# Optimization experiments

Measured on AMD Instinct MI355X. Metric: run time of the kernel, lower is better.

The kernel has to match this reference:

```python
import jax, jax.numpy as jnp
from jax import lax
import numpy as np

P, N, C, S = 16, 128, 256, 64
HID = C // 4  # squeeze_ratio = 4
NEG_SLOPE = 0.01  # nn.LeakyReLU default


def setup_inputs() -> dict:
    key = jax.random.key(0)
    k = jax.random.split(key, 5)
    sc = 0.05
    return {
        "x": jax.random.normal(k[0], (P, N, C, S), jnp.float32),
        "w1a": jax.random.normal(k[1], (P, HID, C, 3), jnp.float32) * sc,
        "w1b": jax.random.normal(k[2], (P, C, HID, 1), jnp.float32) * sc,
        "w3a": jax.random.normal(k[3], (P, HID, C, 3), jnp.float32) * sc,
        "w3b": jax.random.normal(k[4], (P, C, HID, 3), jnp.float32) * sc,
    }


def _conv1d(x, w, pad):
    # x: [n, c_in, s], w: [c_out, c_in, k] -> [n, c_out, s]
    return lax.conv_general_dilated(
        x, w, window_strides=(1,), padding=[(pad, pad)],
        dimension_numbers=("NCH", "OIH", "NCH"))


def _leaky(z):
    return jnp.where(z >= 0, z, NEG_SLOPE * z)


def _avg_pool(x, k, pad):
    # PyTorch AvgPool1d default count_include_pad=True: divide by k everywhere.
    s = lax.reduce_window(x, 0.0, lax.add, (1, 1, k), (1, 1, 1),
                          [(0, 0), (0, 0), (pad, pad)])
    return s / k


def _max_pool(x, k, pad):
    return lax.reduce_window(x, -jnp.inf, lax.max, (1, 1, k), (1, 1, 1),
                             [(0, 0), (0, 0), (pad, pad)])


def reference(x, w1a, w1b, w3a, w3b):
    p, n, c, s = x.shape
    xf = x.reshape(p * n, c, s)

    # 3x1 branch: per-part Conv1d(c->hid,k3,p1) -> LeakyReLU -> Conv1d(hid->c,k1,p0)
    logits3x1 = jax.vmap(
        lambda xi, a, b: _conv1d(_leaky(_conv1d(xi, a, 1)), b, 0))(x, w1a, w1b)
    feat3x1 = (_avg_pool(xf, 3, 1) + _max_pool(xf, 3, 1)).reshape(p, n, c, s)
    feat3x1 = feat3x1 * jax.nn.sigmoid(logits3x1)

    # 3x3 branch: per-part Conv1d(c->hid,k3,p1) -> LeakyReLU -> Conv1d(hid->c,k3,p1)
    logits3x3 = jax.vmap(
        lambda xi, a, b: _conv1d(_leaky(_conv1d(xi, a, 1)), b, 1))(x, w3a, w3b)
    feat3x3 = (_avg_pool(xf, 5, 2) + _max_pool(xf, 5, 2)).reshape(p, n, c, s)
    feat3x3 = feat3x3 * jax.nn.sigmoid(logits3x3)

    # fused temporal max over s -> [p, n, c]
    return jnp.max(feat3x1 + feat3x3, axis=-1)
```

## Files before the change

### kernel.cpp

```cpp
#include <hip/hip_runtime.h>

#define PARTS 16
#define NB 128
#define CH 256
#define SL 64
#define HIDN 64

typedef unsigned short u16;
typedef unsigned short ushort8 __attribute__((ext_vector_type(8)));
typedef unsigned short ushort4v __attribute__((ext_vector_type(4)));
typedef __attribute__((ext_vector_type(8))) short short8v;
typedef __attribute__((ext_vector_type(4))) short short4v;
typedef __attribute__((ext_vector_type(4))) float f32x4;

__device__ __forceinline__ float bf2f(u16 u) {
  union { unsigned u; float f; } t; t.u = ((unsigned)u) << 16; return t.f;
}
__device__ __forceinline__ u16 f2bf(float f) {
  union { float f; unsigned u; } t; t.f = f;
  unsigned u = t.u;
  u += 0x7FFFu + ((u >> 16) & 1u);
  return (u16)(u >> 16);
}

__global__ void cvt_tap(const float* __restrict__ in, u16* __restrict__ out, int NT) {
  const int i = blockIdx.x * 256 + threadIdx.x;
  const int p = i >> 14, xid = i & 16383;
  const float* src = in + (size_t)i * NT;
  for (int t = 0; t < NT; ++t)
    out[(size_t)(p * NT + t) * 16384 + xid] = f2bf(src[t]);
}

#define XROWS 68
#define HROWS 66

__device__ __forceinline__ int xsw(int r, int c) { return (r * 256 + c) ^ ((r & 7) << 3); }
__device__ __forceinline__ int hsw(int r, int c) { return (r * 64 + c) ^ ((r & 7) << 3); }

__global__ __launch_bounds__(256, 2) void tfa_mfma(
    const float* __restrict__ x,
    const u16* __restrict__ wsb,
    float* __restrict__ out)
{
  const u16* W1A = wsb;
  const u16* W3A = wsb + 786432;
  const u16* W1B = wsb + 1572864;
  const u16* W3B = wsb + 1835008;

  __shared__ __attribute__((aligned(16))) u16 xt[XROWS * 256];
  __shared__ __attribute__((aligned(16))) u16 ht1[HROWS * 64];
  __shared__ __attribute__((aligned(16))) u16 ht3[HROWS * 64];

  const int tid = threadIdx.x;
  const int bid = blockIdx.x;
  const int p = bid >> 7;
  const int lane = tid & 63;
  const int w = tid >> 6;

  if (tid < 128) {
    const int rr4 = (tid >> 5);
    const int r = (rr4 == 0) ? 0 : (rr4 == 1) ? 1 : (rr4 == 2) ? 66 : 67;
    const int c = (tid & 31) * 8;
    *(ushort8*)&xt[xsw(r, c)] = (ushort8)0;
  } else if (tid < 160) {
    const int t2 = tid - 128;
    const int r = (t2 & 8) ? 65 : 0;
    const int c = (t2 & 7) * 8;
    u16* b = (t2 & 16) ? ht3 : ht1;
    *(ushort8*)&b[hsw(r, c)] = (ushort8)0;
  }

  {
    const float* xb = x + (size_t)bid * (CH * SL);
    const int s = lane;
    const int r = s + 2;
    #pragma unroll
    for (int j = 0; j < 8; ++j) {
      const int c0 = w * 64 + j * 8;
      ushort8 ov;
      #pragma unroll
      for (int k = 0; k < 8; ++k) ov[k] = f2bf(xb[(c0 + k) * 64 + s]);
      *(ushort8*)&xt[xsw(r, c0)] = ov;
    }
  }
  __syncthreads();

  {
    const int hm = lane & 15;
    const int kg = lane >> 4;
    const int h = w * 16 + hm;
    f32x4 acc1[4], acc3[4];
    #pragma unroll
    for (int nt = 0; nt < 4; ++nt) { acc1[nt] = (f32x4)0.f; acc3[nt] = (f32x4)0.f; }

    #pragma unroll 2
    for (int ks = 0; ks < 8; ++ks) {
      const int kc = ks * 32 + kg * 8;
      short8v a1[3], a3[3];
      #pragma unroll
      for (int t = 0; t < 3; ++t) {
        a1[t] = *(const short8v*)&W1A[(size_t)((p * 3 + t) * 64 + h) * 256 + kc];
        a3[t] = *(const short8v*)&W3A[(size_t)((p * 3 + t) * 64 + h) * 256 + kc];
      }
      #pragma unroll
      for (int nt = 0; nt < 4; ++nt) {
        const int s = nt * 16 + hm;
        #pragma unroll
        for (int t = 0; t < 3; ++t) {
          const int r = s + t + 1;
          const short8v b = *(const short8v*)&xt[xsw(r, kc)];
          acc1[nt] = __builtin_amdgcn_mfma_f32_16x16x32_bf16(a1[t], b, acc1[nt], 0, 0, 0);
          acc3[nt] = __builtin_amdgcn_mfma_f32_16x16x32_bf16(a3[t], b, acc3[nt], 0, 0, 0);
        }
      }
    }

    const int hc = w * 16 + kg * 4;
    #pragma unroll
    for (int nt = 0; nt < 4; ++nt) {
      const int s = nt * 16 + hm;
      const int r = s + 1;
      ushort4v o1, o3;
      #pragma unroll
      for (int q = 0; q < 4; ++q) {
        float v1 = acc1[nt][q]; v1 = v1 >= 0.f ? v1 : 0.01f * v1;
        float v3 = acc3[nt][q]; v3 = v3 >= 0.f ? v3 : 0.01f * v3;
        o1[q] = f2bf(v1); o3[q] = f2bf(v3);
      }
      *(ushort4v*)&ht1[hsw(r, hc)] = o1;
      *(ushort4v*)&ht3[hsw(r, hc)] = o3;
    }
  }
  __syncthreads();

  {
    const int cm = lane & 15;
    const int kg = lane >> 4;

    #pragma unroll
    for (int half = 0; half < 2; ++half) {
      const int mtb = half * 2;
      f32x4 acc[2][4];
      #pragma unroll
      for (int mt = 0; mt < 2; ++mt)
        #pragma unroll
        for (int nt = 0; nt < 4; ++nt) acc[mt][nt] = (f32x4)0.f;

      #pragma unroll
      for (int ks = 0; ks < 2; ++ks) {
        const int kh = ks * 32 + kg * 8;
        short8v a[2];
        #pragma unroll
        for (int mt = 0; mt < 2; ++mt) {
          const int c = w * 64 + (mtb + mt) * 16 + cm;
          a[mt] = *(const short8v*)&W1B[((size_t)p * 256 + c) * 64 + kh];
        }
        #pragma unroll
        for (int nt = 0; nt < 4; ++nt) {
          const int s = nt * 16 + cm;
          const short8v b = *(const short8v*)&ht1[hsw(s + 1, kh)];
          #pragma unroll
          for (int mt = 0; mt < 2; ++mt)
            acc[mt][nt] = __builtin_amdgcn_mfma_f32_16x16x32_bf16(a[mt], b, acc[mt][nt], 0, 0, 0);
        }
      }

      unsigned g1p[2][4][2];
      #pragma unroll
      for (int mt = 0; mt < 2; ++mt)
        #pragma unroll
        for (int nt = 0; nt < 4; ++nt) {
          #pragma unroll
          for (int j = 0; j < 2; ++j) {
            const float ga = 1.f / (1.f + __expf(-acc[mt][nt][2 * j]));
            const float gb = 1.f / (1.f + __expf(-acc[mt][nt][2 * j + 1]));
            g1p[mt][nt][j] = (unsigned)f2bf(ga) | ((unsigned)f2bf(gb) << 16);
          }
          acc[mt][nt] = (f32x4)0.f;
        }

      #pragma unroll
      for (int ks = 0; ks < 2; ++ks) {
        const int kh = ks * 32 + kg * 8;
        #pragma unroll
        for (int t = 0; t < 3; ++t) {
          short8v a[2];
          #pragma unroll
          for (int mt = 0; mt < 2; ++mt) {
            const int c = w * 64 + (mtb + mt) * 16 + cm;
            a[mt] = *(const short8v*)&W3B[(size_t)((p * 3 + t) * 256 + c) * 64 + kh];
          }
          #pragma unroll
          for (int nt = 0; nt < 4; ++nt) {
            const int s = nt * 16 + cm;
            const short8v b = *(const short8v*)&ht3[hsw(s + t, kh)];
            #pragma unroll
            for (int mt = 0; mt < 2; ++mt)
              acc[mt][nt] = __builtin_amdgcn_mfma_f32_16x16x32_bf16(a[mt], b, acc[mt][nt], 0, 0, 0);
          }
        }
      }

      #pragma unroll
      for (int mt = 0; mt < 2; ++mt) {
        const int c4 = w * 64 + (mtb + mt) * 16 + kg * 4;
        float fmx0 = -INFINITY, fmx1 = -INFINITY, fmx2 = -INFINITY, fmx3 = -INFINITY;
        #pragma unroll
        for (int nt = 0; nt < 4; ++nt) {
          const int s = nt * 16 + cm;
          const ushort4v vm2 = *(const ushort4v*)&xt[xsw(s,     c4)];
          const ushort4v vm1 = *(const ushort4v*)&xt[xsw(s + 1, c4)];
          const ushort4v v0  = *(const ushort4v*)&xt[xsw(s + 2, c4)];
          const ushort4v vp1 = *(const ushort4v*)&xt[xsw(s + 3, c4)];
          const ushort4v vp2 = *(const ushort4v*)&xt[xsw(s + 4, c4)];
          const float NI = -INFINITY;
          float ft[4];
          #pragma unroll
          for (int q = 0; q < 4; ++q) {
            const float xm2 = bf2f(vm2[q]), xm1 = bf2f(vm1[q]), x0 = bf2f(v0[q]);
            const float xp1 = bf2f(vp1[q]), xp2 = bf2f(vp2[q]);
            const float mx3 = fmaxf(x0, fmaxf(s >= 1 ? xm1 : NI, s <= 62 ? xp1 : NI));
            const float mx5 = fmaxf(mx3, fmaxf(s >= 2 ? xm2 : NI, s <= 61 ? xp2 : NI));
            const float av3 = (xm1 + x0 + xp1) * (1.f / 3.f);
            const float av5 = (xm2 + xm1 + x0 + xp1 + xp2) * 0.2f;
            const float g1 = bf2f((u16)(g1p[mt][nt][q >> 1] >> ((q & 1) * 16)));
            const float g3 = 1.f / (1.f + __expf(-acc[mt][nt][q]));
            ft[q] = (av3 + mx3) * g1 + (av5 + mx5) * g3;
          }
          fmx0 = fmaxf(fmx0, ft[0]); fmx1 = fmaxf(fmx1, ft[1]);
          fmx2 = fmaxf(fmx2, ft[2]); fmx3 = fmaxf(fmx3, ft[3]);
        }
        #pragma unroll
        for (int off = 1; off < 16; off <<= 1) {
          fmx0 = fmaxf(fmx0, __shfl_xor(fmx0, off));
          fmx1 = fmaxf(fmx1, __shfl_xor(fmx1, off));
          fmx2 = fmaxf(fmx2, __shfl_xor(fmx2, off));
          fmx3 = fmaxf(fmx3, __shfl_xor(fmx3, off));
        }
        if (cm == 0) {
          float4 o; o.x = fmx0; o.y = fmx1; o.z = fmx2; o.w = fmx3;
          *(float4*)&out[(size_t)bid * 256 + c4] = o;
        }
      }
    }
  }
}

#define XROW 72
#define HROW 72

__global__ __launch_bounds__(256, 2) void tfa_kernel(
    const float* __restrict__ x,
    const float* __restrict__ w1a,
    const float* __restrict__ w1b,
    const float* __restrict__ w3a,
    const float* __restrict__ w3b,
    float* __restrict__ out)
{
  __shared__ __attribute__((aligned(16))) u16 x_s[8 + CH * XROW];
  __shared__ __attribute__((aligned(16))) u16 h1_s[8 + HIDN * HROW];
  __shared__ __attribute__((aligned(16))) u16 h3_s[8 + HIDN * HROW];

  const int tid = threadIdx.x;
  const int bid = blockIdx.x;
  const int p = bid >> 7;

  {
    const ushort8 z = {0, 0, 0, 0, 0, 0, 0, 0};
    for (int i = tid; i < 257; i += 256) {
      u16* dst = (i == 0) ? &x_s[0] : &x_s[8 + (i - 1) * XROW + 64];
      *(ushort8*)dst = z;
    }
    if (tid < 65) {
      u16* d1 = (tid == 0) ? &h1_s[0] : &h1_s[8 + (tid - 1) * HROW + 64];
      *(ushort8*)d1 = z;
      u16* d3 = (tid == 0) ? &h3_s[0] : &h3_s[8 + (tid - 1) * HROW + 64];
      *(ushort8*)d3 = z;
    }
  }

  const float* xblk = x + (size_t)bid * (CH * SL);
  #pragma unroll
  for (int j = 0; j < 16; ++j) {
    const int g = tid + 256 * j;
    const float4 v = ((const float4*)xblk)[g];
    const int c = g >> 4, s4 = g & 15;
    ushort4v o;
    o[0] = f2bf(v.x); o[1] = f2bf(v.y); o[2] = f2bf(v.z); o[3] = f2bf(v.w);
    *(ushort4v*)&x_s[8 + c * XROW + s4 * 4] = o;
  }
  __syncthreads();

  {
    const int h = tid >> 2;
    const int sg = tid & 3;
    const int sb = sg << 4;
    float acc1[16], acc3[16];
    #pragma unroll
    for (int i = 0; i < 16; ++i) { acc1[i] = 0.f; acc3[i] = 0.f; }

    const float* w1a_p = w1a + ((size_t)p * HIDN + h) * (CH * 3);
    const float* w3a_p = w3a + ((size_t)p * HIDN + h) * (CH * 3);

    for (int c4 = 0; c4 < CH; c4 += 4) {
      const float4 a0v = *(const float4*)&w1a_p[c4 * 3];
      const float4 a1v = *(const float4*)&w1a_p[c4 * 3 + 4];
      const float4 a2v = *(const float4*)&w1a_p[c4 * 3 + 8];
      const float4 b0v = *(const float4*)&w3a_p[c4 * 3];
      const float4 b1v = *(const float4*)&w3a_p[c4 * 3 + 4];
      const float4 b2v = *(const float4*)&w3a_p[c4 * 3 + 8];
      float wa[12], wb[12];
      wa[0]=a0v.x; wa[1]=a0v.y; wa[2]=a0v.z; wa[3]=a0v.w;
      wa[4]=a1v.x; wa[5]=a1v.y; wa[6]=a1v.z; wa[7]=a1v.w;
      wa[8]=a2v.x; wa[9]=a2v.y; wa[10]=a2v.z; wa[11]=a2v.w;
      wb[0]=b0v.x; wb[1]=b0v.y; wb[2]=b0v.z; wb[3]=b0v.w;
      wb[4]=b1v.x; wb[5]=b1v.y; wb[6]=b1v.z; wb[7]=b1v.w;
      wb[8]=b2v.x; wb[9]=b2v.y; wb[10]=b2v.z; wb[11]=b2v.w;

      #pragma unroll
      for (int cc = 0; cc < 4; ++cc) {
        const int c = c4 + cc;
        const ushort8 w0v = *(const ushort8*)&x_s[c * XROW + sb];
        const ushort8 w1v = *(const ushort8*)&x_s[c * XROW + sb + 8];
        const ushort8 w2v = *(const ushort8*)&x_s[c * XROW + sb + 16];
        const ushort8 w3v = *(const ushort8*)&x_s[c * XROW + sb + 24];
        float xf[19];
        xf[0] = bf2f(w0v[7]);
        #pragma unroll
        for (int d = 0; d < 8; ++d) xf[1 + d] = bf2f(w1v[d]);
        #pragma unroll
        for (int d = 0; d < 8; ++d) xf[9 + d] = bf2f(w2v[d]);
        xf[17] = bf2f(w3v[0]);
        xf[18] = bf2f(w3v[1]);

        const float a0 = wa[cc * 3], a1 = wa[cc * 3 + 1], a2 = wa[cc * 3 + 2];
        const float b0 = wb[cc * 3], b1 = wb[cc * 3 + 1], b2 = wb[cc * 3 + 2];
        #pragma unroll
        for (int i = 0; i < 16; ++i) {
          const float xm = xf[i], x0 = xf[i + 1], xp = xf[i + 2];
          acc1[i] = fmaf(a0, xm, fmaf(a1, x0, fmaf(a2, xp, acc1[i])));
          acc3[i] = fmaf(b0, xm, fmaf(b1, x0, fmaf(b2, xp, acc3[i])));
        }
      }
    }

    ushort8 o1a, o1b, o3a, o3b;
    #pragma unroll
    for (int i = 0; i < 8; ++i) {
      float v1 = acc1[i];     v1 = v1 >= 0.f ? v1 : 0.01f * v1;
      float v3 = acc3[i];     v3 = v3 >= 0.f ? v3 : 0.01f * v3;
      o1a[i] = f2bf(v1); o3a[i] = f2bf(v3);
      float u1 = acc1[i + 8]; u1 = u1 >= 0.f ? u1 : 0.01f * u1;
      float u3 = acc3[i + 8]; u3 = u3 >= 0.f ? u3 : 0.01f * u3;
      o1b[i] = f2bf(u1); o3b[i] = f2bf(u3);
    }
    *(ushort8*)&h1_s[8 + h * HROW + sb]     = o1a;
    *(ushort8*)&h1_s[8 + h * HROW + sb + 8] = o1b;
    *(ushort8*)&h3_s[8 + h * HROW + sb]     = o3a;
    *(ushort8*)&h3_s[8 + h * HROW + sb + 8] = o3b;
  }
  __syncthreads();

  {
    const int lane = tid & 63;
    const int wid = __builtin_amdgcn_readfirstlane(tid >> 6);
    const int s = lane;
    const float* w1b_p = w1b + (size_t)p * (CH * HIDN);
    const float* w3b_p = w3b + (size_t)p * (CH * HIDN * 3);
    float* outp = out + (size_t)bid * CH;

    for (int q = 0; q < 16; ++q) {
      const int c0 = wid * 64 + q * 4;
      float l1[4] = {0.f, 0.f, 0.f, 0.f};
      float l3[4] = {0.f, 0.f, 0.f, 0.f};

      for (int h4 = 0; h4 < HIDN; h4 += 4) {
        float h1v[4], h3a[4], h3b[4], h3c[4];
        #pragma unroll
        for (int u = 0; u < 4; ++u) {
          const int hh = h4 + u;
          h1v[u] = bf2f(h1_s[8 + hh * HROW + s]);
          h3a[u] = bf2f(h3_s[7 + hh * HROW + s]);
          h3b[u] = bf2f(h3_s[8 + hh * HROW + s]);
          h3c[u] = bf2f(h3_s[9 + hh * HROW + s]);
        }
        #pragma unroll
        for (int j = 0; j < 4; ++j) {
          const int c = c0 + j;
          const float4 wv  = *(const float4*)&w1b_p[c * HIDN + h4];
          const float* w3  = &w3b_p[(size_t)(c * HIDN + h4) * 3];
          const float4 w30 = *(const float4*)w3;
          const float4 w31 = *(const float4*)(w3 + 4);
          const float4 w32 = *(const float4*)(w3 + 8);
          float ww[12];
          ww[0]=w30.x; ww[1]=w30.y; ww[2]=w30.z; ww[3]=w30.w;
          ww[4]=w31.x; ww[5]=w31.y; ww[6]=w31.z; ww[7]=w31.w;
          ww[8]=w32.x; ww[9]=w32.y; ww[10]=w32.z; ww[11]=w32.w;
          l1[j] = fmaf(wv.x, h1v[0], fmaf(wv.y, h1v[1],
                  fmaf(wv.z, h1v[2], fmaf(wv.w, h1v[3], l1[j]))));
          #pragma unroll
          for (int u = 0; u < 4; ++u) {
            l3[j] = fmaf(ww[u * 3], h3a[u],
                    fmaf(ww[u * 3 + 1], h3b[u],
                    fmaf(ww[u * 3 + 2], h3c[u], l3[j])));
          }
        }
      }

      #pragma unroll
      for (int j = 0; j < 4; ++j) {
        const int c = c0 + j;
        const u16* xr = &x_s[8 + c * XROW];
        const float xm2 = bf2f(xr[s - 2]);
        const float xm1 = bf2f(xr[s - 1]);
        const float x0  = bf2f(xr[s]);
        const float xp1 = bf2f(xr[s + 1]);
        const float xp2 = bf2f(xr[s + 2]);
        const float NI = -INFINITY;
        const float mx3 = fmaxf(x0, fmaxf(s >= 1 ? xm1 : NI, s <= 62 ? xp1 : NI));
        const float mx5 = fmaxf(mx3, fmaxf(s >= 2 ? xm2 : NI, s <= 61 ? xp2 : NI));
        const float av3 = (xm1 + x0 + xp1) * (1.f / 3.f);
        const float av5 = (xm2 + xm1 + x0 + xp1 + xp2) * 0.2f;
        const float sg1 = 1.f / (1.f + __expf(-l1[j]));
        const float sg3 = 1.f / (1.f + __expf(-l3[j]));
        float feat = (av3 + mx3) * sg1 + (av5 + mx5) * sg3;
        #pragma unroll
        for (int off = 32; off >= 1; off >>= 1)
          feat = fmaxf(feat, __shfl_xor(feat, off));
        if (lane == 0) outp[c] = feat;
      }
    }
  }
}

extern "C" void kernel_launch(void* const* d_in, const int* in_sizes, int n_in,
                              void* d_out, int out_size, void* d_ws, size_t ws_size,
                              hipStream_t stream) {
  (void)in_sizes; (void)n_in; (void)out_size;
  const float* x   = (const float*)d_in[0];
  const float* w1a = (const float*)d_in[1];
  const float* w1b = (const float*)d_in[2];
  const float* w3a = (const float*)d_in[3];
  const float* w3b = (const float*)d_in[4];
  float* out = (float*)d_out;

  const size_t WS_NEED = 2621440ull * 2ull;
  if (ws_size >= WS_NEED) {
    u16* wsb = (u16*)d_ws;
    cvt_tap<<<1024, 256, 0, stream>>>(w1a, wsb,           3);
    cvt_tap<<<1024, 256, 0, stream>>>(w3a, wsb + 786432,  3);
    cvt_tap<<<1024, 256, 0, stream>>>(w1b, wsb + 1572864, 1);
    cvt_tap<<<1024, 256, 0, stream>>>(w3b, wsb + 1835008, 3);
    tfa_mfma<<<PARTS * NB, 256, 0, stream>>>(x, wsb, out);
  } else {
    tfa_kernel<<<PARTS * NB, 256, 0, stream>>>(x, w1a, w1b, w3a, w3b, out);
  }
}
```

Measured before the change: 128.1 us.

## Split MFMA kernel work across 512 threads and use packed bf16 conversion

Doubles the block from 4 to 8 waves. Each phase's work (x load, first conv over time tiles, second conv over channel halves) is split so each wave handles half the previous share, which removes the serial 'half' loop in the second stage. It also swaps the manual float-to-bf16 rounding for the packed __float22bfloat162_rn intrinsic. The intent is more waves in flight to hide global weight-load latency and fewer conversion instructions. The cost is that weight A-fragments are now loaded redundantly by the wave pairs, and occupancy depends on the new launch bounds.

```diff
diff --git a/kernel.cpp b/kernel.cpp
--- a/kernel.cpp
+++ b/kernel.cpp
@@ -1,4 +1,5 @@
 #include <hip/hip_runtime.h>
+#include <hip/hip_bf16.h>
 
 #define PARTS 16
 #define NB 128
@@ -10,7 +11,6 @@
 typedef unsigned short ushort8 __attribute__((ext_vector_type(8)));
 typedef unsigned short ushort4v __attribute__((ext_vector_type(4)));
 typedef __attribute__((ext_vector_type(8))) short short8v;
-typedef __attribute__((ext_vector_type(4))) short short4v;
 typedef __attribute__((ext_vector_type(4))) float f32x4;
 
 __device__ __forceinline__ float bf2f(u16 u) {
@@ -21,6 +21,12 @@
   unsigned u = t.u;
   u += 0x7FFFu + ((u >> 16) & 1u);
   return (u16)(u >> 16);
+}
+__device__ __forceinline__ unsigned pk2bf(float a, float b) {
+  float2 f; f.x = a; f.y = b;
+  union { __hip_bfloat162 h; unsigned u; } cv;
+  cv.h = __float22bfloat162_rn(f);
+  return cv.u;
 }
 
 __global__ void cvt_tap(const float* __restrict__ in, u16* __restrict__ out, int NT) {
@@ -37,7 +43,7 @@
 __device__ __forceinline__ int xsw(int r, int c) { return (r * 256 + c) ^ ((r & 7) << 3); }
 __device__ __forceinline__ int hsw(int r, int c) { return (r * 64 + c) ^ ((r & 7) << 3); }
 
-__global__ __launch_bounds__(256, 2) void tfa_mfma(
+__global__ __launch_bounds__(512, 6) void tfa_mfma(
     const float* __restrict__ x,
     const u16* __restrict__ wsb,
     float* __restrict__ out)
@@ -75,12 +81,16 @@
     const int s = lane;
     const int r = s + 2;
     #pragma unroll
-    for (int j = 0; j < 8; ++j) {
-      const int c0 = w * 64 + j * 8;
-      ushort8 ov;
-      #pragma unroll
-      for (int k = 0; k < 8; ++k) ov[k] = f2bf(xb[(c0 + k) * 64 + s]);
-      *(ushort8*)&xt[xsw(r, c0)] = ov;
+    for (int j = 0; j < 4; ++j) {
+      const int c0 = w * 32 + j * 8;
+      union { ushort8 v; unsigned u[4]; } ov;
+      #pragma unroll
+      for (int k = 0; k < 4; ++k) {
+        const float fa = xb[(c0 + 2 * k) * 64 + s];
+        const float fb = xb[(c0 + 2 * k + 1) * 64 + s];
+        ov.u[k] = pk2bf(fa, fb);
+      }
+      *(ushort8*)&xt[xsw(r, c0)] = ov.v;
     }
   }
   __syncthreads();
@@ -88,10 +98,12 @@
   {
     const int hm = lane & 15;
     const int kg = lane >> 4;
-    const int h = w * 16 + hm;
-    f32x4 acc1[4], acc3[4];
-    #pragma unroll
-    for (int nt = 0; nt < 4; ++nt) { acc1[nt] = (f32x4)0.f; acc3[nt] = (f32x4)0.f; }
+    const int hg = w & 3;
+    const int h = hg * 16 + hm;
+    const int ntb = (w >> 2) * 2;
+    f32x4 acc1[2], acc3[2];
+    #pragma unroll
+    for (int nt = 0; nt < 2; ++nt) { acc1[nt] = (f32x4)0.f; acc3[nt] = (f32x4)0.f; }
 
     #pragma unroll 2
     for (int ks = 0; ks < 8; ++ks) {
@@ -103,8 +115,8 @@
         a3[t] = *(const short8v*)&W3A[(size_t)((p * 3 + t) * 64 + h) * 256 + kc];
       }
       #pragma unroll
-      for (int nt = 0; nt < 4; ++nt) {
-        const int s = nt * 16 + hm;
+      for (int nt = 0; nt < 2; ++nt) {
+        const int s = (ntb + nt) * 16 + hm;
         #pragma unroll
         for (int t = 0; t < 3; ++t) {
           const int r = s + t + 1;
@@ -115,20 +127,22 @@
       }
     }
 
-    const int hc = w * 16 + kg * 4;
-    #pragma unroll
-    for (int nt = 0; nt < 4; ++nt) {
-      const int s = nt * 16 + hm;
+    const int hc = hg * 16 + kg * 4;
+    #pragma unroll
+    for (int nt = 0; nt < 2; ++nt) {
+      const int s = (ntb + nt) * 16 + hm;
       const int r = s + 1;
-      ushort4v o1, o3;
+      float v1[4], v3[4];
       #pragma unroll
       for (int q = 0; q < 4; ++q) {
-        float v1 = acc1[nt][q]; v1 = v1 >= 0.f ? v1 : 0.01f * v1;
-        float v3 = acc3[nt][q]; v3 = v3 >= 0.f ? v3 : 0.01f * v3;
-        o1[q] = f2bf(v1); o3[q] = f2bf(v3);
-      }
-      *(ushort4v*)&ht1[hsw(r, hc)] = o1;
-      *(ushort4v*)&ht3[hsw(r, hc)] = o3;
+        float a = acc1[nt][q]; v1[q] = a >= 0.f ? a : 0.01f * a;
+        float bq = acc3[nt][q]; v3[q] = bq >= 0.f ? bq : 0.01f * bq;
+      }
+      union { ushort4v v; unsigned u[2]; } o1, o3;
+      o1.u[0] = pk2bf(v1[0], v1[1]); o1.u[1] = pk2bf(v1[2], v1[3]);
+      o3.u[0] = pk2bf(v3[0], v3[1]); o3.u[1] = pk2bf(v3[2], v3[3]);
+      *(ushort4v*)&ht1[hsw(r, hc)] = o1.v;
+      *(ushort4v*)&ht3[hsw(r, hc)] = o3.v;
     }
   }
   __syncthreads();
@@ -136,111 +150,109 @@
   {
     const int cm = lane & 15;
     const int kg = lane >> 4;
-
-    #pragma unroll
-    for (int half = 0; half < 2; ++half) {
-      const int mtb = half * 2;
-      f32x4 acc[2][4];
-      #pragma unroll
-      for (int mt = 0; mt < 2; ++mt)
-        #pragma unroll
-        for (int nt = 0; nt < 4; ++nt) acc[mt][nt] = (f32x4)0.f;
-
-      #pragma unroll
-      for (int ks = 0; ks < 2; ++ks) {
-        const int kh = ks * 32 + kg * 8;
+    const int cg = w & 3;
+    const int mtb = (w >> 2) * 2;
+
+    f32x4 acc[2][4];
+    #pragma unroll
+    for (int mt = 0; mt < 2; ++mt)
+      #pragma unroll
+      for (int nt = 0; nt < 4; ++nt) acc[mt][nt] = (f32x4)0.f;
+
+    #pragma unroll
+    for (int ks = 0; ks < 2; ++ks) {
+      const int kh = ks * 32 + kg * 8;
+      short8v a[2];
+      #pragma unroll
+      for (int mt = 0; mt < 2; ++mt) {
+        const int c = cg * 64 + (mtb + mt) * 16 + cm;
+        a[mt] = *(const short8v*)&W1B[((size_t)p * 256 + c) * 64 + kh];
+      }
+      #pragma unroll
+      for (int nt = 0; nt < 4; ++nt) {
+        const int s = nt * 16 + cm;
+        const short8v b = *(const short8v*)&ht1[hsw(s + 1, kh)];
+        #pragma unroll
+        for (int mt = 0; mt < 2; ++mt)
+          acc[mt][nt] = __builtin_amdgcn_mfma_f32_16x16x32_bf16(a[mt], b, acc[mt][nt], 0, 0, 0);
+      }
+    }
+
+    unsigned g1p[2][4][2];
+    #pragma unroll
+    for (int mt = 0; mt < 2; ++mt)
+      #pragma unroll
+      for (int nt = 0; nt < 4; ++nt) {
+        #pragma unroll
+        for (int j = 0; j < 2; ++j) {
+          const float ga = 1.f / (1.f + __expf(-acc[mt][nt][2 * j]));
+          const float gb = 1.f / (1.f + __expf(-acc[mt][nt][2 * j + 1]));
+          g1p[mt][nt][j] = pk2bf(ga, gb);
+        }
+        acc[mt][nt] = (f32x4)0.f;
+      }
+
+    #pragma unroll
+    for (int ks = 0; ks < 2; ++ks) {
+      const int kh = ks * 32 + kg * 8;
+      #pragma unroll
+      for (int t = 0; t < 3; ++t) {
         short8v a[2];
         #pragma unroll
         for (int mt = 0; mt < 2; ++mt) {
-          const int c = w * 64 + (mtb + mt) * 16 + cm;
-          a[mt] = *(const short8v*)&W1B[((size_t)p * 256 + c) * 64 + kh];
+          const int c = cg * 64 + (mtb + mt) * 16 + cm;
+          a[mt] = *(const short8v*)&W3B[(size_t)((p * 3 + t) * 256 + c) * 64 + kh];
         }
         #pragma unroll
         for (int nt = 0; nt < 4; ++nt) {
           const int s = nt * 16 + cm;
-          const short8v b = *(const short8v*)&ht1[hsw(s + 1, kh)];
+          const short8v b = *(const short8v*)&ht3[hsw(s + t, kh)];
           #pragma unroll
           for (int mt = 0; mt < 2; ++mt)
             acc[mt][nt] = __builtin_amdgcn_mfma_f32_16x16x32_bf16(a[mt], b, acc[mt][nt], 0, 0, 0);
         }
       }
-
-      unsigned g1p[2][4][2];
-      #pragma unroll
-      for (int mt = 0; mt < 2; ++mt)
-        #pragma unroll
-        for (int nt = 0; nt < 4; ++nt) {
-          #pragma unroll
-          for (int j = 0; j < 2; ++j) {
-            const float ga = 1.f / (1.f + __expf(-acc[mt][nt][2 * j]));
-            const float gb = 1.f / (1.f + __expf(-acc[mt][nt][2 * j + 1]));
-            g1p[mt][nt][j] = (unsigned)f2bf(ga) | ((unsigned)f2bf(gb) << 16);
-          }
-          acc[mt][nt] = (f32x4)0.f;
-        }
-
-      #pragma unroll
-      for (int ks = 0; ks < 2; ++ks) {
-        const int kh = ks * 32 + kg * 8;
-        #pragma unroll
-        for (int t = 0; t < 3; ++t) {
-          short8v a[2];
-          #pragma unroll
-          for (int mt = 0; mt < 2; ++mt) {
-            const int c = w * 64 + (mtb + mt) * 16 + cm;
-            a[mt] = *(const short8v*)&W3B[(size_t)((p * 3 + t) * 256 + c) * 64 + kh];
-          }
-          #pragma unroll
-          for (int nt = 0; nt < 4; ++nt) {
-            const int s = nt * 16 + cm;
-            const short8v b = *(const short8v*)&ht3[hsw(s + t, kh)];
-            #pragma unroll
-            for (int mt = 0; mt < 2; ++mt)
-              acc[mt][nt] = __builtin_amdgcn_mfma_f32_16x16x32_bf16(a[mt], b, acc[mt][nt], 0, 0, 0);
-          }
-        }
-      }
-
-      #pragma unroll
-      for (int mt = 0; mt < 2; ++mt) {
-        const int c4 = w * 64 + (mtb + mt) * 16 + kg * 4;
-        float fmx0 = -INFINITY, fmx1 = -INFINITY, fmx2 = -INFINITY, fmx3 = -INFINITY;
-        #pragma unroll
-        for (int nt = 0; nt < 4; ++nt) {
-          const int s = nt * 16 + cm;
-          const ushort4v vm2 = *(const ushort4v*)&xt[xsw(s,     c4)];
-          const ushort4v vm1 = *(const ushort4v*)&xt[xsw(s + 1, c4)];
-          const ushort4v v0  = *(const ushort4v*)&xt[xsw(s + 2, c4)];
-          const ushort4v vp1 = *(const ushort4v*)&xt[xsw(s + 3, c4)];
-          const ushort4v vp2 = *(const ushort4v*)&xt[xsw(s + 4, c4)];
-          const float NI = -INFINITY;
-          float ft[4];
-          #pragma unroll
-          for (int q = 0; q < 4; ++q) {
-            const float xm2 = bf2f(vm2[q]), xm1 = bf2f(vm1[q]), x0 = bf2f(v0[q]);
-            const float xp1 = bf2f(vp1[q]), xp2 = bf2f(vp2[q]);
-            const float mx3 = fmaxf(x0, fmaxf(s >= 1 ? xm1 : NI, s <= 62 ? xp1 : NI));
-            const float mx5 = fmaxf(mx3, fmaxf(s >= 2 ? xm2 : NI, s <= 61 ? xp2 : NI));
-            const float av3 = (xm1 + x0 + xp1) * (1.f / 3.f);
-            const float av5 = (xm2 + xm1 + x0 + xp1 + xp2) * 0.2f;
-            const float g1 = bf2f((u16)(g1p[mt][nt][q >> 1] >> ((q & 1) * 16)));
-            const float g3 = 1.f / (1.f + __expf(-acc[mt][nt][q]));
-            ft[q] = (av3 + mx3) * g1 + (av5 + mx5) * g3;
-          }
-          fmx0 = fmaxf(fmx0, ft[0]); fmx1 = fmaxf(fmx1, ft[1]);
-          fmx2 = fmaxf(fmx2, ft[2]); fmx3 = fmaxf(fmx3, ft[3]);
-        }
-        #pragma unroll
-        for (int off = 1; off < 16; off <<= 1) {
-          fmx0 = fmaxf(fmx0, __shfl_xor(fmx0, off));
-          fmx1 = fmaxf(fmx1, __shfl_xor(fmx1, off));
-          fmx2 = fmaxf(fmx2, __shfl_xor(fmx2, off));
-          fmx3 = fmaxf(fmx3, __shfl_xor(fmx3, off));
-        }
-        if (cm == 0) {
-          float4 o; o.x = fmx0; o.y = fmx1; o.z = fmx2; o.w = fmx3;
-          *(float4*)&out[(size_t)bid * 256 + c4] = o;
-        }
+    }
+
+    #pragma unroll
+    for (int mt = 0; mt < 2; ++mt) {
+      const int c4 = cg * 64 + (mtb + mt) * 16 + kg * 4;
+      float fmx0 = -INFINITY, fmx1 = -INFINITY, fmx2 = -INFINITY, fmx3 = -INFINITY;
+      #pragma unroll
+      for (int nt = 0; nt < 4; ++nt) {
+        const int s = nt * 16 + cm;
+        const ushort4v vm2 = *(const ushort4v*)&xt[xsw(s,     c4)];
+        const ushort4v vm1 = *(const ushort4v*)&xt[xsw(s + 1, c4)];
+        const ushort4v v0  = *(const ushort4v*)&xt[xsw(s + 2, c4)];
+        const ushort4v vp1 = *(const ushort4v*)&xt[xsw(s + 3, c4)];
+        const ushort4v vp2 = *(const ushort4v*)&xt[xsw(s + 4, c4)];
+        const float NI = -INFINITY;
+        float ft[4];
+        #pragma unroll
+        for (int q = 0; q < 4; ++q) {
+          const float xm2 = bf2f(vm2[q]), xm1 = bf2f(vm1[q]), x0 = bf2f(v0[q]);
+          const float xp1 = bf2f(vp1[q]), xp2 = bf2f(vp2[q]);
+          const float mx3 = fmaxf(x0, fmaxf(s >= 1 ? xm1 : NI, s <= 62 ? xp1 : NI));
+          const float mx5 = fmaxf(mx3, fmaxf(s >= 2 ? xm2 : NI, s <= 61 ? xp2 : NI));
+          const float av3 = (xm1 + x0 + xp1) * (1.f / 3.f);
+          const float av5 = (xm2 + xm1 + x0 + xp1 + xp2) * 0.2f;
+          const float g1 = bf2f((u16)(g1p[mt][nt][q >> 1] >> ((q & 1) * 16)));
+          const float g3 = 1.f / (1.f + __expf(-acc[mt][nt][q]));
+          ft[q] = (av3 + mx3) * g1 + (av5 + mx5) * g3;
+        }
+        fmx0 = fmaxf(fmx0, ft[0]); fmx1 = fmaxf(fmx1, ft[1]);
+        fmx2 = fmaxf(fmx2, ft[2]); fmx3 = fmaxf(fmx3, ft[3]);
+      }
+      #pragma unroll
+      for (int off = 1; off < 16; off <<= 1) {
+        fmx0 = fmaxf(fmx0, __shfl_xor(fmx0, off));
+        fmx1 = fmaxf(fmx1, __shfl_xor(fmx1, off));
+        fmx2 = fmaxf(fmx2, __shfl_xor(fmx2, off));
+        fmx3 = fmaxf(fmx3, __shfl_xor(fmx3, off));
+      }
+      if (cm == 0) {
+        float4 o; o.x = fmx0; o.y = fmx1; o.z = fmx2; o.w = fmx3;
+        *(float4*)&out[(size_t)bid * 256 + c4] = o;
       }
     }
   }
@@ -451,7 +463,7 @@
     cvt_tap<<<1024, 256, 0, stream>>>(w3a, wsb + 786432,  3);
     cvt_tap<<<1024, 256, 0, stream>>>(w1b, wsb + 1572864, 1);
     cvt_tap<<<1024, 256, 0, stream>>>(w3b, wsb + 1835008, 3);
-    tfa_mfma<<<PARTS * NB, 256, 0, stream>>>(x, wsb, out);
+    tfa_mfma<<<PARTS * NB, 512, 0, stream>>>(x, wsb, out);
   } else {
     tfa_kernel<<<PARTS * NB, 256, 0, stream>>>(x, w1a, w1b, w3a, w3b, out);
   }
```

New measurement: 203.5 us. 1.59x slower.

## Shrink LDS footprint with single hidden buffer and no halo rows for higher occupancy

Applied to the files above, without the earlier changes.

The kernel drops the padded halo rows from the x and hidden tiles and handles boundaries by clamping indices and zeroing out-of-range operands. It keeps one shared hidden buffer, holding the 3x3 hidden activations in registers until the 1x1 gate pass finishes, then reuses the buffer. It precomputes all 1x1 sigmoid gates before the 3x3 second conv, raises launch bounds to 4 blocks per CU, and uses packed bf16 conversion. The aim is higher occupancy through less LDS, at the cost of more registers held across phases, extra barriers and extra select work.

```diff
diff --git a/kernel.cpp b/kernel.cpp
--- a/kernel.cpp
+++ b/kernel.cpp
@@ -1,4 +1,5 @@
 #include <hip/hip_runtime.h>
+#include <hip/hip_bf16.h>
 
 #define PARTS 16
 #define NB 128
@@ -7,10 +8,10 @@
 #define HIDN 64
 
 typedef unsigned short u16;
+typedef unsigned int u32;
 typedef unsigned short ushort8 __attribute__((ext_vector_type(8)));
 typedef unsigned short ushort4v __attribute__((ext_vector_type(4)));
 typedef __attribute__((ext_vector_type(8))) short short8v;
-typedef __attribute__((ext_vector_type(4))) short short4v;
 typedef __attribute__((ext_vector_type(4))) float f32x4;
 
 __device__ __forceinline__ float bf2f(u16 u) {
@@ -21,6 +22,12 @@
   unsigned u = t.u;
   u += 0x7FFFu + ((u >> 16) & 1u);
   return (u16)(u >> 16);
+}
+__device__ __forceinline__ unsigned pk2bf(float a, float b) {
+  float2 f; f.x = a; f.y = b;
+  union { __hip_bfloat162 h; unsigned u; } cv;
+  cv.h = __float22bfloat162_rn(f);
+  return cv.u;
 }
 
 __global__ void cvt_tap(const float* __restrict__ in, u16* __restrict__ out, int NT) {
@@ -31,13 +38,10 @@
     out[(size_t)(p * NT + t) * 16384 + xid] = f2bf(src[t]);
 }
 
-#define XROWS 68
-#define HROWS 66
-
 __device__ __forceinline__ int xsw(int r, int c) { return (r * 256 + c) ^ ((r & 7) << 3); }
 __device__ __forceinline__ int hsw(int r, int c) { return (r * 64 + c) ^ ((r & 7) << 3); }
 
-__global__ __launch_bounds__(256, 2) void tfa_mfma(
+__global__ __launch_bounds__(256, 4) void tfa_mfma(
     const float* __restrict__ x,
     const u16* __restrict__ wsb,
     float* __restrict__ out)
@@ -47,9 +51,8 @@
   const u16* W1B = wsb + 1572864;
   const u16* W3B = wsb + 1835008;
 
-  __shared__ __attribute__((aligned(16))) u16 xt[XROWS * 256];
-  __shared__ __attribute__((aligned(16))) u16 ht1[HROWS * 64];
-  __shared__ __attribute__((aligned(16))) u16 ht3[HROWS * 64];
+  __shared__ __attribute__((aligned(16))) u16 xt[64 * 256];
+  __shared__ __attribute__((aligned(16))) u16 ht[64 * 64];
 
   const int tid = threadIdx.x;
   const int bid = blockIdx.x;
@@ -57,38 +60,30 @@
   const int lane = tid & 63;
   const int w = tid >> 6;
 
-  if (tid < 128) {
-    const int rr4 = (tid >> 5);
-    const int r = (rr4 == 0) ? 0 : (rr4 == 1) ? 1 : (rr4 == 2) ? 66 : 67;
-    const int c = (tid & 31) * 8;
-    *(ushort8*)&xt[xsw(r, c)] = (ushort8)0;
-  } else if (tid < 160) {
-    const int t2 = tid - 128;
-    const int r = (t2 & 8) ? 65 : 0;
-    const int c = (t2 & 7) * 8;
-    u16* b = (t2 & 16) ? ht3 : ht1;
-    *(ushort8*)&b[hsw(r, c)] = (ushort8)0;
-  }
-
   {
     const float* xb = x + (size_t)bid * (CH * SL);
     const int s = lane;
-    const int r = s + 2;
     #pragma unroll
     for (int j = 0; j < 8; ++j) {
       const int c0 = w * 64 + j * 8;
-      ushort8 ov;
-      #pragma unroll
-      for (int k = 0; k < 8; ++k) ov[k] = f2bf(xb[(c0 + k) * 64 + s]);
-      *(ushort8*)&xt[xsw(r, c0)] = ov;
-    }
-  }
-  __syncthreads();
-
-  {
-    const int hm = lane & 15;
-    const int kg = lane >> 4;
-    const int h = w * 16 + hm;
+      union { ushort8 v; unsigned u[4]; } ov;
+      #pragma unroll
+      for (int k = 0; k < 4; ++k) {
+        const float fa = xb[(c0 + 2 * k) * 64 + s];
+        const float fb = xb[(c0 + 2 * k + 1) * 64 + s];
+        ov.u[k] = pk2bf(fa, fb);
+      }
+      *(ushort8*)&xt[xsw(s, c0)] = ov.v;
+    }
+  }
+  __syncthreads();
+
+  const int cm = lane & 15;
+  const int kg = lane >> 4;
+
+  u32 H3pk[4][2];
+  {
+    const int h = w * 16 + cm;
     f32x4 acc1[4], acc3[4];
     #pragma unroll
     for (int nt = 0; nt < 4; ++nt) { acc1[nt] = (f32x4)0.f; acc3[nt] = (f32x4)0.f; }
@@ -104,11 +99,13 @@
       }
       #pragma unroll
       for (int nt = 0; nt < 4; ++nt) {
-        const int s = nt * 16 + hm;
+        const int s = nt * 16 + cm;
         #pragma unroll
         for (int t = 0; t < 3; ++t) {
-          const int r = s + t + 1;
-          const short8v b = *(const short8v*)&xt[xsw(r, kc)];
+          const int r = s + t - 1;
+          const bool oob = (unsigned)r > 63u;
+          const short8v bb = *(const short8v*)&xt[xsw(oob ? s : r, kc)];
+          const short8v b = oob ? (short8v)(short)0 : bb;
           acc1[nt] = __builtin_amdgcn_mfma_f32_16x16x32_bf16(a1[t], b, acc1[nt], 0, 0, 0);
           acc3[nt] = __builtin_amdgcn_mfma_f32_16x16x32_bf16(a3[t], b, acc3[nt], 0, 0, 0);
         }
@@ -118,129 +115,154 @@
     const int hc = w * 16 + kg * 4;
     #pragma unroll
     for (int nt = 0; nt < 4; ++nt) {
-      const int s = nt * 16 + hm;
-      const int r = s + 1;
-      ushort4v o1, o3;
+      const int s = nt * 16 + cm;
+      float v1[4], v3[4];
       #pragma unroll
       for (int q = 0; q < 4; ++q) {
-        float v1 = acc1[nt][q]; v1 = v1 >= 0.f ? v1 : 0.01f * v1;
-        float v3 = acc3[nt][q]; v3 = v3 >= 0.f ? v3 : 0.01f * v3;
-        o1[q] = f2bf(v1); o3[q] = f2bf(v3);
-      }
-      *(ushort4v*)&ht1[hsw(r, hc)] = o1;
-      *(ushort4v*)&ht3[hsw(r, hc)] = o3;
-    }
-  }
-  __syncthreads();
-
-  {
-    const int cm = lane & 15;
-    const int kg = lane >> 4;
-
-    #pragma unroll
-    for (int half = 0; half < 2; ++half) {
-      const int mtb = half * 2;
-      f32x4 acc[2][4];
-      #pragma unroll
-      for (int mt = 0; mt < 2; ++mt)
-        #pragma unroll
-        for (int nt = 0; nt < 4; ++nt) acc[mt][nt] = (f32x4)0.f;
-
-      #pragma unroll
-      for (int ks = 0; ks < 2; ++ks) {
-        const int kh = ks * 32 + kg * 8;
+        const float a = acc1[nt][q]; v1[q] = a >= 0.f ? a : 0.01f * a;
+        const float bq = acc3[nt][q]; v3[q] = bq >= 0.f ? bq : 0.01f * bq;
+      }
+      union { ushort4v v; u32 u[2]; } o1;
+      o1.u[0] = pk2bf(v1[0], v1[1]); o1.u[1] = pk2bf(v1[2], v1[3]);
+      *(ushort4v*)&ht[hsw(s, hc)] = o1.v;
+      H3pk[nt][0] = pk2bf(v3[0], v3[1]); H3pk[nt][1] = pk2bf(v3[2], v3[3]);
+    }
+  }
+  __syncthreads();
+
+  u32 g1p[4][4][2];
+  #pragma unroll
+  for (int half = 0; half < 2; ++half) {
+    f32x4 acc[2][4];
+    #pragma unroll
+    for (int mt = 0; mt < 2; ++mt)
+      #pragma unroll
+      for (int nt = 0; nt < 4; ++nt) acc[mt][nt] = (f32x4)0.f;
+
+    #pragma unroll
+    for (int ks = 0; ks < 2; ++ks) {
+      const int kh = ks * 32 + kg * 8;
+      short8v a[2];
+      #pragma unroll
+      for (int mt = 0; mt < 2; ++mt) {
+        const int c = w * 64 + (half * 2 + mt) * 16 + cm;
+        a[mt] = *(const short8v*)&W1B[((size_t)p * 256 + c) * 64 + kh];
+      }
+      #pragma unroll
+      for (int nt = 0; nt < 4; ++nt) {
+        const int s = nt * 16 + cm;
+        const short8v b = *(const short8v*)&ht[hsw(s, kh)];
+        #pragma unroll
+        for (int mt = 0; mt < 2; ++mt)
+          acc[mt][nt] = __builtin_amdgcn_mfma_f32_16x16x32_bf16(a[mt], b, acc[mt][nt], 0, 0, 0);
+      }
+    }
+    #pragma unroll
+    for (int mt = 0; mt < 2; ++mt)
+      #pragma unroll
+      for (int nt = 0; nt < 4; ++nt) {
+        #pragma unroll
+        for (int j = 0; j < 2; ++j) {
+          const float ga = 1.f / (1.f + __expf(-acc[mt][nt][2 * j]));
+          const float gb = 1.f / (1.f + __expf(-acc[mt][nt][2 * j + 1]));
+          g1p[half * 2 + mt][nt][j] = pk2bf(ga, gb);
+        }
+      }
+  }
+  __syncthreads();
+
+  {
+    const int hc = w * 16 + kg * 4;
+    #pragma unroll
+    for (int nt = 0; nt < 4; ++nt) {
+      const int s = nt * 16 + cm;
+      union { ushort4v v; u32 u[2]; } o3;
+      o3.u[0] = H3pk[nt][0]; o3.u[1] = H3pk[nt][1];
+      *(ushort4v*)&ht[hsw(s, hc)] = o3.v;
+    }
+  }
+  __syncthreads();
+
+  #pragma unroll 1
+  for (int half = 0; half < 2; ++half) {
+    f32x4 acc[2][4];
+    #pragma unroll
+    for (int mt = 0; mt < 2; ++mt)
+      #pragma unroll
+      for (int nt = 0; nt < 4; ++nt) acc[mt][nt] = (f32x4)0.f;
+
+    #pragma unroll
+    for (int ks = 0; ks < 2; ++ks) {
+      const int kh = ks * 32 + kg * 8;
+      #pragma unroll
+      for (int t = 0; t < 3; ++t) {
         short8v a[2];
         #pragma unroll
         for (int mt = 0; mt < 2; ++mt) {
-          const int c = w * 64 + (mtb + mt) * 16 + cm;
-          a[mt] = *(const short8v*)&W1B[((size_t)p * 256 + c) * 64 + kh];
+          const int c = w * 64 + (half * 2 + mt) * 16 + cm;
+          a[mt] = *(const short8v*)&W3B[(size_t)((p * 3 + t) * 256 + c) * 64 + kh];
         }
         #pragma unroll
         for (int nt = 0; nt < 4; ++nt) {
           const int s = nt * 16 + cm;
-          const short8v b = *(const short8v*)&ht1[hsw(s + 1, kh)];
+          const int r = s + t - 1;
+          const bool oob = (unsigned)r > 63u;
+          const short8v bb = *(const short8v*)&ht[hsw(oob ? s : r, kh)];
+          const short8v b = oob ? (short8v)(short)0 : bb;
           #pragma unroll
           for (int mt = 0; mt < 2; ++mt)
             acc[mt][nt] = __builtin_amdgcn_mfma_f32_16x16x32_bf16(a[mt], b, acc[mt][nt], 0, 0, 0);
         }
       }
-
-      unsigned g1p[2][4][2];
-      #pragma unroll
-      for (int mt = 0; mt < 2; ++mt)
-        #pragma unroll
-        for (int nt = 0; nt < 4; ++nt) {
-          #pragma unroll
-          for (int j = 0; j < 2; ++j) {
-            const float ga = 1.f / (1.f + __expf(-acc[mt][nt][2 * j]));
-            const float gb = 1.f / (1.f + __expf(-acc[mt][nt][2 * j + 1]));
-            g1p[mt][nt][j] = (unsigned)f2bf(ga) | ((unsigned)f2bf(gb) << 16);
-          }
-          acc[mt][nt] = (f32x4)0.f;
-        }
-
-      #pragma unroll
-      for (int ks = 0; ks < 2; ++ks) {
-        const int kh = ks * 32 + kg * 8;
-        #pragma unroll
-        for (int t = 0; t < 3; ++t) {
-          short8v a[2];
-          #pragma unroll
-          for (int mt = 0; mt < 2; ++mt) {
-            const int c = w * 64 + (mtb + mt) * 16 + cm;
-            a[mt] = *(const short8v*)&W3B[(size_t)((p * 3 + t) * 256 + c) * 64 + kh];
-          }
-          #pragma unroll
-          for (int nt = 0; nt < 4; ++nt) {
-            const int s = nt * 16 + cm;
-            const short8v b = *(const short8v*)&ht3[hsw(s + t, kh)];
-            #pragma unroll
-            for (int mt = 0; mt < 2; ++mt)
-              acc[mt][nt] = __builtin_amdgcn_mfma_f32_16x16x32_bf16(a[mt], b, acc[mt][nt], 0, 0, 0);
-          }
-        }
-      }
-
-      #pragma unroll
-      for (int mt = 0; mt < 2; ++mt) {
-        const int c4 = w * 64 + (mtb + mt) * 16 + kg * 4;
-        float fmx0 = -INFINITY, fmx1 = -INFINITY, fmx2 = -INFINITY, fmx3 = -INFINITY;
-        #pragma unroll
-        for (int nt = 0; nt < 4; ++nt) {
-          const int s = nt * 16 + cm;
-          const ushort4v vm2 = *(const ushort4v*)&xt[xsw(s,     c4)];
-          const ushort4v vm1 = *(const ushort4v*)&xt[xsw(s + 1, c4)];
-          const ushort4v v0  = *(const ushort4v*)&xt[xsw(s + 2, c4)];
-          const ushort4v vp1 = *(const ushort4v*)&xt[xsw(s + 3, c4)];
-          const ushort4v vp2 = *(const ushort4v*)&xt[xsw(s + 4, c4)];
-          const float NI = -INFINITY;
-          float ft[4];
-          #pragma unroll
-          for (int q = 0; q < 4; ++q) {
-            const float xm2 = bf2f(vm2[q]), xm1 = bf2f(vm1[q]), x0 = bf2f(v0[q]);
-            const float xp1 = bf2f(vp1[q]), xp2 = bf2f(vp2[q]);
-            const float mx3 = fmaxf(x0, fmaxf(s >= 1 ? xm1 : NI, s <= 62 ? xp1 : NI));
-            const float mx5 = fmaxf(mx3, fmaxf(s >= 2 ? xm2 : NI, s <= 61 ? xp2 : NI));
-            const float av3 = (xm1 + x0 + xp1) * (1.f / 3.f);
-            const float av5 = (xm2 + xm1 + x0 + xp1 + xp2) * 0.2f;
-            const float g1 = bf2f((u16)(g1p[mt][nt][q >> 1] >> ((q & 1) * 16)));
-            const float g3 = 1.f / (1.f + __expf(-acc[mt][nt][q]));
-            ft[q] = (av3 + mx3) * g1 + (av5 + mx5) * g3;
-          }
-          fmx0 = fmaxf(fmx0, ft[0]); fmx1 = fmaxf(fmx1, ft[1]);
-          fmx2 = fmaxf(fmx2, ft[2]); fmx3 = fmaxf(fmx3, ft[3]);
-        }
-        #pragma unroll
-        for (int off = 1; off < 16; off <<= 1) {
-          fmx0 = fmaxf(fmx0, __shfl_xor(fmx0, off));
-          fmx1 = fmaxf(fmx1, __shfl_xor(fmx1, off));
-          fmx2 = fmaxf(fmx2, __shfl_xor(fmx2, off));
-          fmx3 = fmaxf(fmx3, __shfl_xor(fmx3, off));
-        }
-        if (cm == 0) {
-          float4 o; o.x = fmx0; o.y = fmx1; o.z = fmx2; o.w = fmx3;
-          *(float4*)&out[(size_t)bid * 256 + c4] = o;
-        }
+    }
+
+    #pragma unroll
+    for (int mt = 0; mt < 2; ++mt) {
+      const int c4 = w * 64 + (half * 2 + mt) * 16 + kg * 4;
+      float fmx0 = -INFINITY, fmx1 = -INFINITY, fmx2 = -INFINITY, fmx3 = -INFINITY;
+      #pragma unroll
+      for (int nt = 0; nt < 4; ++nt) {
+        const int sg = nt * 16 + cm;
+        const int rm2 = sg >= 2 ? sg - 2 : 0;
+        const int rm1 = sg >= 1 ? sg - 1 : 0;
+        const int rp1 = sg <= 62 ? sg + 1 : 63;
+        const int rp2 = sg <= 61 ? sg + 2 : 63;
+        const ushort4v vm2 = *(const ushort4v*)&xt[xsw(rm2, c4)];
+        const ushort4v vm1 = *(const ushort4v*)&xt[xsw(rm1, c4)];
+        const ushort4v v0  = *(const ushort4v*)&xt[xsw(sg,  c4)];
+        const ushort4v vp1 = *(const ushort4v*)&xt[xsw(rp1, c4)];
+        const ushort4v vp2 = *(const ushort4v*)&xt[xsw(rp2, c4)];
+        const float NI = -INFINITY;
+        float ft[4];
+        #pragma unroll
+        for (int q = 0; q < 4; ++q) {
+          const float xm2r = bf2f(vm2[q]), xm1r = bf2f(vm1[q]), x0 = bf2f(v0[q]);
+          const float xp1r = bf2f(vp1[q]), xp2r = bf2f(vp2[q]);
+          const float am2 = sg >= 2 ? xm2r : 0.f;
+          const float am1 = sg >= 1 ? xm1r : 0.f;
+          const float ap1 = sg <= 62 ? xp1r : 0.f;
+          const float ap2 = sg <= 61 ? xp2r : 0.f;
+          const float mx3 = fmaxf(x0, fmaxf(sg >= 1 ? xm1r : NI, sg <= 62 ? xp1r : NI));
+          const float mx5 = fmaxf(mx3, fmaxf(sg >= 2 ? xm2r : NI, sg <= 61 ? xp2r : NI));
+          const float av3 = (am1 + x0 + ap1) * (1.f / 3.f);
+          const float av5 = (am2 + am1 + x0 + ap1 + ap2) * 0.2f;
+          const float g1 = bf2f((u16)(g1p[half * 2 + mt][nt][q >> 1] >> ((q & 1) * 16)));
+          const float g3 = 1.f / (1.f + __expf(-acc[mt][nt][q]));
+          ft[q] = (av3 + mx3) * g1 + (av5 + mx5) * g3;
+        }
+        fmx0 = fmaxf(fmx0, ft[0]); fmx1 = fmaxf(fmx1, ft[1]);
+        fmx2 = fmaxf(fmx2, ft[2]); fmx3 = fmaxf(fmx3, ft[3]);
+      }
+      #pragma unroll
+      for (int off = 1; off < 16; off <<= 1) {
+        fmx0 = fmaxf(fmx0, __shfl_xor(fmx0, off));
+        fmx1 = fmaxf(fmx1, __shfl_xor(fmx1, off));
+        fmx2 = fmaxf(fmx2, __shfl_xor(fmx2, off));
+        fmx3 = fmaxf(fmx3, __shfl_xor(fmx3, off));
+      }
+      if (cm == 0) {
+        float4 o; o.x = fmx0; o.y = fmx1; o.z = fmx2; o.w = fmx3;
+        *(float4*)&out[(size_t)bid * 256 + c4] = o;
       }
     }
   }
```

Result: slower. 222.5 us (+73.7%).
